# Performance work log

Measured on AMD Instinct MI355X. Metric: run time of the kernel, lower is better.

Reference implementation:

```python
import jax, jax.numpy as jnp
import numpy as np

B, T, C, H = 4, 2048, 1024, 16
D = C // H

def setup_inputs() -> dict:
    key = jax.random.key(0)
    ks = jax.random.split(key, 9)
    s = 0.02
    return {
        "x": jax.random.normal(ks[0], (B, T, C), dtype=jnp.float32),
        "Wq": jax.random.normal(ks[1], (C, C), dtype=jnp.float32) * s,
        "bq": jnp.zeros((C,), dtype=jnp.float32),
        "Wk": jax.random.normal(ks[2], (C, C), dtype=jnp.float32) * s,
        "bk": jnp.zeros((C,), dtype=jnp.float32),
        "Wv": jax.random.normal(ks[3], (C, C), dtype=jnp.float32) * s,
        "bv": jnp.zeros((C,), dtype=jnp.float32),
        "Wo": jax.random.normal(ks[4], (C, C), dtype=jnp.float32) * s,
        "bo": jnp.zeros((C,), dtype=jnp.float32),
    }

def reference(x, Wq, bq, Wk, bk, Wv, bv, Wo, bo):
    # torch nn.Linear: y = x @ W.T + b
    q = x @ Wq.T + bq  # (B,T,C)
    k = x @ Wk.T + bk
    v = x @ Wv.T + bv
    # (B,H,T,D)
    q = q.reshape(B, T, H, D).transpose(0, 2, 1, 3)
    k = k.reshape(B, T, H, D).transpose(0, 2, 1, 3)
    v = v.reshape(B, T, H, D).transpose(0, 2, 1, 3)
    scale = 1.0 / jnp.sqrt(jnp.asarray(D, dtype=q.dtype))
    att = jnp.einsum("bhqd,bhkd->bhqk", q, k) * scale  # (B,H,T,T)
    causal = jnp.tril(jnp.ones((T, T), dtype=bool))
    att = jnp.where(causal[None, None], att, jnp.asarray(-jnp.inf, dtype=att.dtype))
    att = jax.nn.softmax(att, axis=-1)
    y = jnp.einsum("bhqk,bhkd->bhqd", att, v)  # (B,H,T,D)
    y = y.transpose(0, 2, 1, 3).reshape(B, T, C)
    return y @ Wo.T + bo
```

## Files before the change

kernel.cpp:

```cpp
#include <hip/hip_runtime.h>
#include <hip/hip_bf16.h>
#include <stdint.h>

typedef unsigned short u16;
typedef __bf16 bf16x8 __attribute__((ext_vector_type(8)));
typedef float f32x4 __attribute__((ext_vector_type(4)));
typedef float f32x16 __attribute__((ext_vector_type(16)));

#define NB 4
#define NT 2048
#define NC 1024
#define NH 16
#define ND 64
#define NM 8192
#define KVB 64

__device__ __forceinline__ u16 f2bf(float f) {
  union { float f; uint32_t u; } v; v.f = f;
  return (u16)((v.u + 0x7FFFu + ((v.u >> 16) & 1u)) >> 16);
}

__device__ __forceinline__ uint32_t pk2(float a, float b) {
  union { __hip_bfloat162 h; uint32_t u; } c;
  c.h = __float22bfloat162_rn(float2{a, b});
  return c.u;
}

__device__ __forceinline__ float fexp2(float x) {
#if __has_builtin(__builtin_amdgcn_exp2f)
  return __builtin_amdgcn_exp2f(x);
#else
  return exp2f(x);
#endif
}

__device__ __forceinline__ void g2l16(const void* g, void* l) {
  __builtin_amdgcn_global_load_lds((__attribute__((address_space(1))) const void*)g,
                                   (__attribute__((address_space(3))) void*)l,
                                   16, 0, 0);
}

__global__ __launch_bounds__(256) void cvt4(const float* __restrict__ in,
                                            u16* __restrict__ out, int n4) {
  int i = blockIdx.x * 256 + threadIdx.x;
  if (i >= n4) return;
  float4 v = ((const float4*)in)[i];
  ushort4 o;
  o.x = f2bf(v.x); o.y = f2bf(v.y); o.z = f2bf(v.z); o.w = f2bf(v.w);
  ((ushort4*)out)[i] = o;
}

template <int EPI>
__global__ __launch_bounds__(512, 2) void gemmP(
    const u16* __restrict__ A,
    const u16* __restrict__ W0, const u16* __restrict__ W1, const u16* __restrict__ W2,
    const float* __restrict__ b0, const float* __restrict__ b1, const float* __restrict__ b2,
    void* o0, void* o1, void* o2, int M, int N, int K) {
  const int z = blockIdx.z;
  const u16* Bw = (z == 0) ? W0 : ((z == 1) ? W1 : W2);
  const float* bias = (z == 0) ? b0 : ((z == 1) ? b1 : b2);
  void* outp = (z == 0) ? o0 : ((z == 1) ? o1 : o2);

  __shared__ __align__(16) char SB[3 * 49152];

  const int nbn = N >> 7;
  const int lb = (blockIdx.x & 7) * (gridDim.x >> 3) + (blockIdx.x >> 3);
  const int m0 = (lb / nbn) << 8;
  const int n0 = (lb % nbn) << 7;
  const int t = threadIdx.x;
  const int wid = t >> 6, lane = t & 63;
  const int wm = wid >> 1, wn = wid & 1;
  const int lo = lane & 15, hi = lane >> 4;

  const int arow0 = t >> 3;
  const int acol = (((t & 7) ^ (arow0 & 7)) << 3);
  const u16* Asrc0 = A + (size_t)(m0 + arow0) * K + acol;
  const u16* Bsrc0 = Bw + (size_t)(n0 + arow0) * K + acol;
  const int ldsoff = t * 16;

  f32x4 acc[4][4];
#pragma unroll
  for (int f = 0; f < 4; ++f)
#pragma unroll
    for (int g = 0; g < 4; ++g) acc[f][g] = f32x4{0.f, 0.f, 0.f, 0.f};

  const int NTILES = K >> 6;

  auto STAGE = [&](int buf, int kt) {
    char* Ad = SB + buf * 49152 + ldsoff;
    char* Bd = SB + buf * 49152 + 32768 + ldsoff;
    const u16* As = Asrc0 + kt * 64;
    const u16* Bs = Bsrc0 + kt * 64;
#pragma unroll
    for (int j = 0; j < 4; ++j) g2l16(As + (size_t)(j << 6) * K, Ad + j * 8192);
#pragma unroll
    for (int j = 0; j < 2; ++j) g2l16(Bs + (size_t)(j << 6) * K, Bd + j * 8192);
  };

  STAGE(0, 0);
  STAGE(1, 1);

  int cur = 0;
  for (int kt = 0; kt < NTILES; ++kt) {
    if (kt == NTILES - 1)
      asm volatile("s_waitcnt vmcnt(0)" ::: "memory");
    else
      asm volatile("s_waitcnt vmcnt(6)" ::: "memory");
    __builtin_amdgcn_sched_barrier(0);
    __builtin_amdgcn_s_barrier();
    __builtin_amdgcn_sched_barrier(0);

    if (kt + 2 < NTILES) {
      int nb = cur + 2;
      if (nb >= 3) nb -= 3;
      STAGE(nb, kt + 2);
    }

    const char* Ab = SB + cur * 49152;
    const char* Bb = SB + cur * 49152 + 32768;
    bf16x8 af[2][4], bfr[2][4];
#pragma unroll
    for (int kh = 0; kh < 2; ++kh) {
      const int slot = ((kh << 2) | hi) ^ (lo & 7);
#pragma unroll
      for (int f = 0; f < 4; ++f)
        af[kh][f] = *(const bf16x8*)(Ab + (wm * 64 + f * 16 + lo) * 128 + slot * 16);
#pragma unroll
      for (int g = 0; g < 4; ++g)
        bfr[kh][g] = *(const bf16x8*)(Bb + (wn * 64 + g * 16 + lo) * 128 + slot * 16);
    }
    __builtin_amdgcn_s_setprio(1);
#pragma unroll
    for (int kh = 0; kh < 2; ++kh)
#pragma unroll
      for (int f = 0; f < 4; ++f)
#pragma unroll
        for (int g = 0; g < 4; ++g)
          acc[f][g] = __builtin_amdgcn_mfma_f32_16x16x32_bf16(af[kh][f], bfr[kh][g],
                                                              acc[f][g], 0, 0, 0);
    __builtin_amdgcn_s_setprio(0);
    cur = (cur + 1 == 3) ? 0 : cur + 1;
  }

  const float scl = (EPI == 0 && z == 0) ? 0.125f * 1.44269504089f : 1.0f;
#pragma unroll
  for (int f = 0; f < 4; ++f) {
#pragma unroll
    for (int g = 0; g < 4; ++g) {
#pragma unroll
      for (int r = 0; r < 4; ++r) {
        const int rg = m0 + wm * 64 + f * 16 + hi * 4 + r;
        const int cg = n0 + wn * 64 + g * 16 + lo;
        const float v = (acc[f][g][r] + bias[cg]) * scl;
        if (EPI == 0) {
          const int bb = rg >> 11, tt = rg & (NT - 1);
          const int hh = cg >> 6, dd = cg & (ND - 1);
          size_t idx;
          if (z == 2)
            idx = ((size_t)(bb * NH + hh) * ND + dd) * NT + tt;
          else
            idx = ((size_t)(bb * NH + hh) * NT + tt) * ND + dd;
          ((u16*)outp)[idx] = f2bf(v);
        } else {
          ((float*)outp)[(size_t)rg * N + cg] = v;
        }
      }
    }
  }
}

__global__ __launch_bounds__(512, 4) void flash5(const u16* __restrict__ Q,
                                                 const u16* __restrict__ Kg,
                                                 const u16* __restrict__ Vtg,
                                                 u16* __restrict__ Y) {
  __shared__ __align__(16) char LDS[65536];

  const int n = blockIdx.x;
  const int xcd = n & 7, slot = n >> 3;
  const int bh = (xcd << 3) | (slot >> 3);
  const int pt = slot & 7;
  const int qtB = 15 - pt;
  const int bb = bh >> 4, hh = bh & (NH - 1);
  const int tid = threadIdx.x;
  const int lane = tid & 63;
  const int grp = tid >> 8;
  const int ws4 = (tid >> 6) & 3;
  const int ql = lane & 31, h5 = lane >> 5;
  const int swz = (ql & 7) << 4;

  const u16* Qb = Q + (size_t)bh * NT * ND;
  const u16* Kb = Kg + (size_t)bh * NT * ND;
  const u16* Vb = Vtg + (size_t)bh * ND * NT;

  const int ntA = 2 * pt + 2;
  const int kvb1 = 15 - 2 * pt;
  const int q0wB = (qtB << 7) + (ws4 << 5);

  int q0w = grp ? q0wB : (pt << 7) + (ws4 << 5);
  int qg = q0w + ql;

  bf16x8 qf[4];
#pragma unroll
  for (int s = 0; s < 4; ++s)
    qf[s] = *(const bf16x8*)(Qb + (size_t)qg * ND + s * 16 + h5 * 8);

  f32x16 O0 = 0.f, O1 = 0.f;
  float lr = 0.f;

  const int tl = tid & 255;
  char* myL = LDS + (grp << 15);

  auto kvof = [&](int it) {
    return grp ? (kvb1 + it) : (it < ntA ? it : it - ntA);
  };

  auto STAGE = [&](int buf, int kv) {
#pragma unroll
    for (int p = 0; p < 2; ++p) {
      const int c = tl + (p << 8);
      const int row = c >> 3;
      const int so = ((c & 7) << 4) ^ ((row & 7) << 4);
      g2l16((const char*)(Kb + (size_t)((kv << 6) + row) * ND) + so,
            myL + (buf << 14) + c * 16);
      g2l16((const char*)(Vb + (size_t)row * NT + (kv << 6)) + so,
            myL + (buf << 14) + 8192 + c * 16);
    }
  };

  auto WRITEY = [&](const f32x16& A0, const f32x16& A1, float inv, int qgl) {
    u16* Yb = Y + ((size_t)bb * NT + qgl) * NC + hh * ND;
#pragma unroll
    for (int rq = 0; rq < 16; rq += 4) {
      const int dbase = 2 * rq + 4 * h5;
      uint2 w2;
      w2.x = pk2(A0[rq] * inv, A0[rq + 1] * inv);
      w2.y = pk2(A0[rq + 2] * inv, A0[rq + 3] * inv);
      *(uint2*)(Yb + dbase) = w2;
      w2.x = pk2(A1[rq] * inv, A1[rq + 1] * inv);
      w2.y = pk2(A1[rq + 2] * inv, A1[rq + 3] * inv);
      *(uint2*)(Yb + 32 + dbase) = w2;
    }
  };

  STAGE(0, kvof(0));
  __syncthreads();

  for (int it = 0; it < 17; ++it) {
    const int buf = it & 1;
    if (it < 16) STAGE(buf ^ 1, kvof(it + 1));

    if (!grp && it == ntA) {
      const float lt = lr + __shfl_xor(lr, 32, 64);
      WRITEY(O0, O1, 1.f / lt, qg);
      O0 = 0.f; O1 = 0.f; lr = 0.f;
      q0w = q0wB; qg = q0w + ql;
#pragma unroll
      for (int s = 0; s < 4; ++s)
        qf[s] = *(const bf16x8*)(Qb + (size_t)qg * ND + s * 16 + h5 * 8);
    }

    const int kv0 = kvof(it) << 6;
    const char* Kc = myL + (buf << 14);
    const char* Vc = Kc + 8192;

    f32x16 Sa0 = 0.f, Sa1 = 0.f;
    __builtin_amdgcn_s_setprio(1);
#pragma unroll
    for (int s = 0; s < 4; ++s) {
      bf16x8 kf0 = *(const bf16x8*)(Kc + ql * 128 + ((s * 32 + h5 * 16) ^ swz));
      bf16x8 kf1 = *(const bf16x8*)(Kc + (32 + ql) * 128 + ((s * 32 + h5 * 16) ^ swz));
      Sa0 = __builtin_amdgcn_mfma_f32_32x32x16_bf16(kf0, qf[s], Sa0, 0, 0, 0);
      Sa1 = __builtin_amdgcn_mfma_f32_32x32x16_bf16(kf1, qf[s], Sa1, 0, 0, 0);
    }
    __builtin_amdgcn_s_setprio(0);

    if (kv0 + 63 > q0w) {
#pragma unroll
      for (int r = 0; r < 16; ++r) {
        const int kvb = kv0 + (r & 3) + 8 * (r >> 2) + 4 * h5;
        if (kvb > qg) Sa0[r] = -3e38f;
        if (kvb + 32 > qg) Sa1[r] = -3e38f;
      }
    }

    float t0 = 0.f, t1 = 0.f, t2 = 0.f, t3 = 0.f;
#pragma unroll
    for (int r = 0; r < 16; r += 4) {
      const float a0 = fexp2(Sa0[r]),     a1 = fexp2(Sa0[r + 1]);
      const float a2 = fexp2(Sa0[r + 2]), a3 = fexp2(Sa0[r + 3]);
      const float b0 = fexp2(Sa1[r]),     b1 = fexp2(Sa1[r + 1]);
      const float b2 = fexp2(Sa1[r + 2]), b3 = fexp2(Sa1[r + 3]);
      Sa0[r] = a0; Sa0[r + 1] = a1; Sa0[r + 2] = a2; Sa0[r + 3] = a3;
      Sa1[r] = b0; Sa1[r + 1] = b1; Sa1[r + 2] = b2; Sa1[r + 3] = b3;
      t0 += a0 + b0; t1 += a1 + b1; t2 += a2 + b2; t3 += a3 + b3;
    }
    lr += (t0 + t1) + (t2 + t3);

    __builtin_amdgcn_s_setprio(1);
#pragma unroll
    for (int ks = 0; ks < 4; ++ks) {
      const int k0 = ks & 1;
      const f32x16& Sk = (ks < 2) ? Sa0 : Sa1;
      const uint32_t a0 = pk2(Sk[8 * k0],     Sk[8 * k0 + 1]);
      const uint32_t a1 = pk2(Sk[8 * k0 + 2], Sk[8 * k0 + 3]);
      const uint32_t b0 = pk2(Sk[8 * k0 + 4], Sk[8 * k0 + 5]);
      const uint32_t b1 = pk2(Sk[8 * k0 + 6], Sk[8 * k0 + 7]);
      const uint32_t c0 = h5 ? b0 : a0, c1 = h5 ? b1 : a1;
      const uint32_t d0 = h5 ? a0 : b0, d1 = h5 ? a1 : b1;
      const uint32_t x0 = __shfl_xor(d0, 32, 64);
      const uint32_t x1 = __shfl_xor(d1, 32, 64);
      union { uint32_t u[4]; bf16x8 v; } pf;
      pf.u[0] = h5 ? x0 : c0;
      pf.u[1] = h5 ? x1 : c1;
      pf.u[2] = h5 ? c0 : x0;
      pf.u[3] = h5 ? c1 : x1;
      bf16x8 vf0 = *(const bf16x8*)(Vc + ql * 128 + ((ks * 32 + h5 * 16) ^ swz));
      bf16x8 vf1 = *(const bf16x8*)(Vc + (32 + ql) * 128 + ((ks * 32 + h5 * 16) ^ swz));
      O0 = __builtin_amdgcn_mfma_f32_32x32x16_bf16(vf0, pf.v, O0, 0, 0, 0);
      O1 = __builtin_amdgcn_mfma_f32_32x32x16_bf16(vf1, pf.v, O1, 0, 0, 0);
    }
    __builtin_amdgcn_s_setprio(0);

    __syncthreads();
  }

  const int cslot = (ws4 << 6) + lane;
  char* cb = LDS + cslot * 136;
  if (!grp) {
#pragma unroll
    for (int j = 0; j < 8; ++j) {
      *(float2*)(cb + j * 8)      = float2{O0[2 * j], O0[2 * j + 1]};
      *(float2*)(cb + 64 + j * 8) = float2{O1[2 * j], O1[2 * j + 1]};
    }
    *(float*)(cb + 128) = lr;
  }
  __syncthreads();
  if (grp) {
#pragma unroll
    for (int j = 0; j < 8; ++j) {
      const float2 u = *(const float2*)(cb + j * 8);
      const float2 v = *(const float2*)(cb + 64 + j * 8);
      O0[2 * j] += u.x; O0[2 * j + 1] += u.y;
      O1[2 * j] += v.x; O1[2 * j + 1] += v.y;
    }
    lr += *(const float*)(cb + 128);
    const float lt = lr + __shfl_xor(lr, 32, 64);
    WRITEY(O0, O1, 1.f / lt, qg);
  }
}

extern "C" void kernel_launch(void* const* d_in, const int* in_sizes, int n_in,
                              void* d_out, int out_size, void* d_ws, size_t ws_size,
                              hipStream_t stream) {
  const float* x  = (const float*)d_in[0];
  const float* Wq = (const float*)d_in[1];
  const float* bq = (const float*)d_in[2];
  const float* Wk = (const float*)d_in[3];
  const float* bk = (const float*)d_in[4];
  const float* Wv = (const float*)d_in[5];
  const float* bv = (const float*)d_in[6];
  const float* Wo = (const float*)d_in[7];
  const float* bo = (const float*)d_in[8];

  const size_t SZ_X = (size_t)NM * NC * 2;
  const size_t SZ_W = (size_t)NC * NC * 2;
  char* ws = (char*)d_ws;
  u16* xb  = (u16*)ws;
  u16* wqb = (u16*)(ws + SZ_X);
  u16* wkb = (u16*)(ws + SZ_X + 1 * SZ_W);
  u16* wvb = (u16*)(ws + SZ_X + 2 * SZ_W);
  u16* wob = (u16*)(ws + SZ_X + 3 * SZ_W);
  u16* vb  = (u16*)(ws + SZ_X + 4 * SZ_W);
  u16* yb  = (u16*)(ws + 2 * SZ_X + 4 * SZ_W);
  u16* qb = (u16*)d_out;
  u16* kb = (u16*)((char*)d_out + SZ_X);

  if (ws_size < 3 * SZ_X + 4 * SZ_W) return;

  cvt4<<<dim3(NM * NC / 4 / 256), 256, 0, stream>>>(x, xb, NM * NC / 4);
  cvt4<<<dim3(NC * NC / 4 / 256), 256, 0, stream>>>(Wq, wqb, NC * NC / 4);
  cvt4<<<dim3(NC * NC / 4 / 256), 256, 0, stream>>>(Wk, wkb, NC * NC / 4);
  cvt4<<<dim3(NC * NC / 4 / 256), 256, 0, stream>>>(Wv, wvb, NC * NC / 4);
  cvt4<<<dim3(NC * NC / 4 / 256), 256, 0, stream>>>(Wo, wob, NC * NC / 4);

  gemmP<0><<<dim3(256, 1, 3), 512, 0, stream>>>(
      xb, wqb, wkb, wvb, bq, bk, bv, qb, kb, vb, NM, NC, NC);

  flash5<<<dim3(512), 512, 0, stream>>>(qb, kb, vb, yb);

  gemmP<1><<<dim3(256, 1, 1), 512, 0, stream>>>(
      yb, wob, wob, wob, bo, bo, bo, d_out, d_out, d_out, NM, NC, NC);
}
```

Baseline: 165.5 us.

## Interleave async LDS prefetch with two k-half MFMA phases and flatten QKV grid

The GEMM main loop is split into two k-half phases separated by an extra barrier. Each phase issues half of the next-next tile's global-to-LDS loads right after its own LDS fragment reads, so global traffic is spread across the MFMA work instead of issued in one burst. The QKV projection grid is also flattened from a 3D launch into a 1D grid of 768 blocks, with the weight matrix (z) folded into the XCD-swizzled tile index so all three projections share A-tile locality. K and N become compile-time constants. The extra barrier per tile adds synchronization cost.

Result: slower. 171.1 us (+3.4%).

```diff
diff --git a/kernel.cpp b/kernel.cpp
--- a/kernel.cpp
+++ b/kernel.cpp
@@ -51,22 +51,24 @@
 }
 
 template <int EPI>
-__global__ __launch_bounds__(512, 2) void gemmP(
+__global__ __launch_bounds__(512, 2) void gemmF(
     const u16* __restrict__ A,
     const u16* __restrict__ W0, const u16* __restrict__ W1, const u16* __restrict__ W2,
     const float* __restrict__ b0, const float* __restrict__ b1, const float* __restrict__ b2,
-    void* o0, void* o1, void* o2, int M, int N, int K) {
-  const int z = blockIdx.z;
+    void* o0, void* o1, void* o2) {
+  constexpr int K = NC;
+  __shared__ __align__(16) char SB[3 * 49152];
+
+  const int ntn = gridDim.x >> 5;
+  const int lb = (blockIdx.x & 7) * (gridDim.x >> 3) + (blockIdx.x >> 3);
+  const int m0 = (lb / ntn) << 8;
+  const int nt = lb % ntn;
+  const int z = nt >> 3;
+  const int n0 = (nt & 7) << 7;
   const u16* Bw = (z == 0) ? W0 : ((z == 1) ? W1 : W2);
   const float* bias = (z == 0) ? b0 : ((z == 1) ? b1 : b2);
   void* outp = (z == 0) ? o0 : ((z == 1) ? o1 : o2);
 
-  __shared__ __align__(16) char SB[3 * 49152];
-
-  const int nbn = N >> 7;
-  const int lb = (blockIdx.x & 7) * (gridDim.x >> 3) + (blockIdx.x >> 3);
-  const int m0 = (lb / nbn) << 8;
-  const int n0 = (lb % nbn) << 7;
   const int t = threadIdx.x;
   const int wid = t >> 6, lane = t & 63;
   const int wm = wid >> 1, wn = wid & 1;
@@ -86,7 +88,7 @@
 
   const int NTILES = K >> 6;
 
-  auto STAGE = [&](int buf, int kt) {
+  auto STAGE_FULL = [&](int buf, int kt) {
     char* Ad = SB + buf * 49152 + ldsoff;
     char* Bd = SB + buf * 49152 + 32768 + ldsoff;
     const u16* As = Asrc0 + kt * 64;
@@ -97,8 +99,8 @@
     for (int j = 0; j < 2; ++j) g2l16(Bs + (size_t)(j << 6) * K, Bd + j * 8192);
   };
 
-  STAGE(0, 0);
-  STAGE(1, 1);
+  STAGE_FULL(0, 0);
+  STAGE_FULL(1, 1);
 
   int cur = 0;
   for (int kt = 0; kt < NTILES; ++kt) {
@@ -107,38 +109,69 @@
     else
       asm volatile("s_waitcnt vmcnt(6)" ::: "memory");
     __builtin_amdgcn_sched_barrier(0);
-    __builtin_amdgcn_s_barrier();
+    asm volatile("s_barrier" ::: "memory");
     __builtin_amdgcn_sched_barrier(0);
-
-    if (kt + 2 < NTILES) {
-      int nb = cur + 2;
-      if (nb >= 3) nb -= 3;
-      STAGE(nb, kt + 2);
-    }
 
     const char* Ab = SB + cur * 49152;
     const char* Bb = SB + cur * 49152 + 32768;
-    bf16x8 af[2][4], bfr[2][4];
-#pragma unroll
-    for (int kh = 0; kh < 2; ++kh) {
-      const int slot = ((kh << 2) | hi) ^ (lo & 7);
+    int nb = cur + 2;
+    if (nb >= 3) nb -= 3;
+    char* Ad = SB + nb * 49152 + ldsoff;
+    char* Bd = SB + nb * 49152 + 32768 + ldsoff;
+    const u16* As = Asrc0 + (kt + 2) * 64;
+    const u16* Bs = Bsrc0 + (kt + 2) * 64;
+    const bool st = (kt + 2 < NTILES);
+
+    {
+      const int ksl = 0;
+      const int slot = ((ksl << 2) | hi) ^ (lo & 7);
+      bf16x8 af[4], bfr[4];
 #pragma unroll
       for (int f = 0; f < 4; ++f)
-        af[kh][f] = *(const bf16x8*)(Ab + (wm * 64 + f * 16 + lo) * 128 + slot * 16);
+        af[f] = *(const bf16x8*)(Ab + (wm * 64 + f * 16 + lo) * 128 + slot * 16);
 #pragma unroll
       for (int g = 0; g < 4; ++g)
-        bfr[kh][g] = *(const bf16x8*)(Bb + (wn * 64 + g * 16 + lo) * 128 + slot * 16);
-    }
-    __builtin_amdgcn_s_setprio(1);
-#pragma unroll
-    for (int kh = 0; kh < 2; ++kh)
+        bfr[g] = *(const bf16x8*)(Bb + (wn * 64 + g * 16 + lo) * 128 + slot * 16);
+      if (st) {
+        g2l16(As + (size_t)(0 << 6) * K, Ad + 0 * 8192);
+        g2l16(As + (size_t)(1 << 6) * K, Ad + 1 * 8192);
+        g2l16(Bs + (size_t)(0 << 6) * K, Bd + 0 * 8192);
+      }
+      __builtin_amdgcn_s_setprio(1);
 #pragma unroll
       for (int f = 0; f < 4; ++f)
 #pragma unroll
         for (int g = 0; g < 4; ++g)
-          acc[f][g] = __builtin_amdgcn_mfma_f32_16x16x32_bf16(af[kh][f], bfr[kh][g],
+          acc[f][g] = __builtin_amdgcn_mfma_f32_16x16x32_bf16(af[f], bfr[g],
                                                               acc[f][g], 0, 0, 0);
-    __builtin_amdgcn_s_setprio(0);
+      __builtin_amdgcn_s_setprio(0);
+    }
+    asm volatile("s_barrier" ::: "memory");
+
+    {
+      const int ksl = 1;
+      const int slot = ((ksl << 2) | hi) ^ (lo & 7);
+      bf16x8 af[4], bfr[4];
+#pragma unroll
+      for (int f = 0; f < 4; ++f)
+        af[f] = *(const bf16x8*)(Ab + (wm * 64 + f * 16 + lo) * 128 + slot * 16);
+#pragma unroll
+      for (int g = 0; g < 4; ++g)
+        bfr[g] = *(const bf16x8*)(Bb + (wn * 64 + g * 16 + lo) * 128 + slot * 16);
+      if (st) {
+        g2l16(As + (size_t)(2 << 6) * K, Ad + 2 * 8192);
+        g2l16(As + (size_t)(3 << 6) * K, Ad + 3 * 8192);
+        g2l16(Bs + (size_t)(1 << 6) * K, Bd + 1 * 8192);
+      }
+      __builtin_amdgcn_s_setprio(1);
+#pragma unroll
+      for (int f = 0; f < 4; ++f)
+#pragma unroll
+        for (int g = 0; g < 4; ++g)
+          acc[f][g] = __builtin_amdgcn_mfma_f32_16x16x32_bf16(af[f], bfr[g],
+                                                              acc[f][g], 0, 0, 0);
+      __builtin_amdgcn_s_setprio(0);
+    }
     cur = (cur + 1 == 3) ? 0 : cur + 1;
   }
 
@@ -162,7 +195,7 @@
             idx = ((size_t)(bb * NH + hh) * NT + tt) * ND + dd;
           ((u16*)outp)[idx] = f2bf(v);
         } else {
-          ((float*)outp)[(size_t)rg * N + cg] = v;
+          ((float*)outp)[(size_t)rg * NC + cg] = v;
         }
       }
     }
@@ -383,11 +416,11 @@
   cvt4<<<dim3(NC * NC / 4 / 256), 256, 0, stream>>>(Wv, wvb, NC * NC / 4);
   cvt4<<<dim3(NC * NC / 4 / 256), 256, 0, stream>>>(Wo, wob, NC * NC / 4);
 
-  gemmP<0><<<dim3(256, 1, 3), 512, 0, stream>>>(
-      xb, wqb, wkb, wvb, bq, bk, bv, qb, kb, vb, NM, NC, NC);
+  gemmF<0><<<dim3(768), 512, 0, stream>>>(
+      xb, wqb, wkb, wvb, bq, bk, bv, qb, kb, vb);
 
   flash5<<<dim3(512), 512, 0, stream>>>(qb, kb, vb, yb);
 
-  gemmP<1><<<dim3(256, 1, 1), 512, 0, stream>>>(
-      yb, wob, wob, wob, bo, bo, bo, d_out, d_out, d_out, NM, NC, NC);
-}
+  gemmF<1><<<dim3(256), 512, 0, stream>>>(
+      yb, wob, wob, wob, bo, bo, bo, d_out, d_out, d_out);
+}
```

## Shrink GEMM tiles to 128x128x32 for higher occupancy and merge weight conversions

Applied to the files above, without the earlier changes.

The projection GEMMs move from 256x128 tiles with K-step 64 (144KB LDS, 2 blocks/CU) to 128x128 tiles with K-step 32 (48KB LDS), using a 2x4 wave layout, a new XOR swizzle, and twice as many blocks. The goal is more resident blocks per CU and better load balance across the grid, so that latency is hidden through occupancy. The cost is less data reuse per tile and more barriers per unit of work. Separately, the four weight-conversion launches become one kernel with a 2D grid, which removes launch overhead.

Result: slower. 171.3 us (+3.5%).

```diff
diff --git a/kernel.cpp b/kernel.cpp
--- a/kernel.cpp
+++ b/kernel.cpp
@@ -50,8 +50,23 @@
   ((ushort4*)out)[i] = o;
 }
 
+__global__ __launch_bounds__(256) void cvtW(const float* __restrict__ w0,
+                                            const float* __restrict__ w1,
+                                            const float* __restrict__ w2,
+                                            const float* __restrict__ w3,
+                                            u16* o0, u16* o1, u16* o2, u16* o3) {
+  const int y = blockIdx.y;
+  const float* in = (y == 0) ? w0 : (y == 1) ? w1 : (y == 2) ? w2 : w3;
+  u16* out = (y == 0) ? o0 : (y == 1) ? o1 : (y == 2) ? o2 : o3;
+  int i = blockIdx.x * 256 + threadIdx.x;
+  float4 v = ((const float4*)in)[i];
+  ushort4 o;
+  o.x = f2bf(v.x); o.y = f2bf(v.y); o.z = f2bf(v.z); o.w = f2bf(v.w);
+  ((ushort4*)out)[i] = o;
+}
+
 template <int EPI>
-__global__ __launch_bounds__(512, 2) void gemmP(
+__global__ __launch_bounds__(512, 6) void gemmQ(
     const u16* __restrict__ A,
     const u16* __restrict__ W0, const u16* __restrict__ W1, const u16* __restrict__ W2,
     const float* __restrict__ b0, const float* __restrict__ b1, const float* __restrict__ b2,
@@ -61,40 +76,34 @@
   const float* bias = (z == 0) ? b0 : ((z == 1) ? b1 : b2);
   void* outp = (z == 0) ? o0 : ((z == 1) ? o1 : o2);
 
-  __shared__ __align__(16) char SB[3 * 49152];
+  __shared__ __align__(16) char SB[3 * 16384];
 
   const int nbn = N >> 7;
   const int lb = (blockIdx.x & 7) * (gridDim.x >> 3) + (blockIdx.x >> 3);
-  const int m0 = (lb / nbn) << 8;
+  const int m0 = (lb / nbn) << 7;
   const int n0 = (lb % nbn) << 7;
   const int t = threadIdx.x;
   const int wid = t >> 6, lane = t & 63;
-  const int wm = wid >> 1, wn = wid & 1;
+  const int wm = wid >> 2, wn = wid & 3;
   const int lo = lane & 15, hi = lane >> 4;
 
-  const int arow0 = t >> 3;
-  const int acol = (((t & 7) ^ (arow0 & 7)) << 3);
-  const u16* Asrc0 = A + (size_t)(m0 + arow0) * K + acol;
-  const u16* Bsrc0 = Bw + (size_t)(n0 + arow0) * K + acol;
+  const int rw = t >> 2;
+  const int chs = (((t & 3) ^ (rw & 3) ^ ((rw >> 2) & 3)) << 3);
+  const u16* Asrc0 = A + (size_t)(m0 + rw) * K + chs;
+  const u16* Bsrc0 = Bw + (size_t)(n0 + rw) * K + chs;
   const int ldsoff = t * 16;
 
-  f32x4 acc[4][4];
+  f32x4 acc[4][2];
 #pragma unroll
   for (int f = 0; f < 4; ++f)
 #pragma unroll
-    for (int g = 0; g < 4; ++g) acc[f][g] = f32x4{0.f, 0.f, 0.f, 0.f};
-
-  const int NTILES = K >> 6;
+    for (int g = 0; g < 2; ++g) acc[f][g] = f32x4{0.f, 0.f, 0.f, 0.f};
+
+  const int NTILES = K >> 5;
 
   auto STAGE = [&](int buf, int kt) {
-    char* Ad = SB + buf * 49152 + ldsoff;
-    char* Bd = SB + buf * 49152 + 32768 + ldsoff;
-    const u16* As = Asrc0 + kt * 64;
-    const u16* Bs = Bsrc0 + kt * 64;
-#pragma unroll
-    for (int j = 0; j < 4; ++j) g2l16(As + (size_t)(j << 6) * K, Ad + j * 8192);
-#pragma unroll
-    for (int j = 0; j < 2; ++j) g2l16(Bs + (size_t)(j << 6) * K, Bd + j * 8192);
+    g2l16(Asrc0 + kt * 32, SB + buf * 16384 + ldsoff);
+    g2l16(Bsrc0 + kt * 32, SB + buf * 16384 + 8192 + ldsoff);
   };
 
   STAGE(0, 0);
@@ -105,9 +114,9 @@
     if (kt == NTILES - 1)
       asm volatile("s_waitcnt vmcnt(0)" ::: "memory");
     else
-      asm volatile("s_waitcnt vmcnt(6)" ::: "memory");
+      asm volatile("s_waitcnt vmcnt(2)" ::: "memory");
     __builtin_amdgcn_sched_barrier(0);
-    __builtin_amdgcn_s_barrier();
+    asm volatile("s_barrier" ::: "memory");
     __builtin_amdgcn_sched_barrier(0);
 
     if (kt + 2 < NTILES) {
@@ -116,28 +125,26 @@
       STAGE(nb, kt + 2);
     }
 
-    const char* Ab = SB + cur * 49152;
-    const char* Bb = SB + cur * 49152 + 32768;
-    bf16x8 af[2][4], bfr[2][4];
-#pragma unroll
-    for (int kh = 0; kh < 2; ++kh) {
-      const int slot = ((kh << 2) | hi) ^ (lo & 7);
-#pragma unroll
-      for (int f = 0; f < 4; ++f)
-        af[kh][f] = *(const bf16x8*)(Ab + (wm * 64 + f * 16 + lo) * 128 + slot * 16);
-#pragma unroll
-      for (int g = 0; g < 4; ++g)
-        bfr[kh][g] = *(const bf16x8*)(Bb + (wn * 64 + g * 16 + lo) * 128 + slot * 16);
+    const char* Ab = SB + cur * 16384;
+    const char* Bb = SB + cur * 16384 + 8192;
+    bf16x8 af[4], bfr[2];
+#pragma unroll
+    for (int f = 0; f < 4; ++f) {
+      const int row = wm * 64 + f * 16 + lo;
+      af[f] = *(const bf16x8*)(Ab + row * 64 + ((hi ^ (row & 3) ^ ((row >> 2) & 3)) << 4));
+    }
+#pragma unroll
+    for (int g = 0; g < 2; ++g) {
+      const int row = wn * 32 + g * 16 + lo;
+      bfr[g] = *(const bf16x8*)(Bb + row * 64 + ((hi ^ (row & 3) ^ ((row >> 2) & 3)) << 4));
     }
     __builtin_amdgcn_s_setprio(1);
 #pragma unroll
-    for (int kh = 0; kh < 2; ++kh)
-#pragma unroll
-      for (int f = 0; f < 4; ++f)
-#pragma unroll
-        for (int g = 0; g < 4; ++g)
-          acc[f][g] = __builtin_amdgcn_mfma_f32_16x16x32_bf16(af[kh][f], bfr[kh][g],
-                                                              acc[f][g], 0, 0, 0);
+    for (int f = 0; f < 4; ++f)
+#pragma unroll
+      for (int g = 0; g < 2; ++g)
+        acc[f][g] = __builtin_amdgcn_mfma_f32_16x16x32_bf16(af[f], bfr[g],
+                                                            acc[f][g], 0, 0, 0);
     __builtin_amdgcn_s_setprio(0);
     cur = (cur + 1 == 3) ? 0 : cur + 1;
   }
@@ -146,11 +153,11 @@
 #pragma unroll
   for (int f = 0; f < 4; ++f) {
 #pragma unroll
-    for (int g = 0; g < 4; ++g) {
+    for (int g = 0; g < 2; ++g) {
 #pragma unroll
       for (int r = 0; r < 4; ++r) {
         const int rg = m0 + wm * 64 + f * 16 + hi * 4 + r;
-        const int cg = n0 + wn * 64 + g * 16 + lo;
+        const int cg = n0 + wn * 32 + g * 16 + lo;
         const float v = (acc[f][g][r] + bias[cg]) * scl;
         if (EPI == 0) {
           const int bb = rg >> 11, tt = rg & (NT - 1);
@@ -378,16 +385,14 @@
   if (ws_size < 3 * SZ_X + 4 * SZ_W) return;
 
   cvt4<<<dim3(NM * NC / 4 / 256), 256, 0, stream>>>(x, xb, NM * NC / 4);
-  cvt4<<<dim3(NC * NC / 4 / 256), 256, 0, stream>>>(Wq, wqb, NC * NC / 4);
-  cvt4<<<dim3(NC * NC / 4 / 256), 256, 0, stream>>>(Wk, wkb, NC * NC / 4);
-  cvt4<<<dim3(NC * NC / 4 / 256), 256, 0, stream>>>(Wv, wvb, NC * NC / 4);
-  cvt4<<<dim3(NC * NC / 4 / 256), 256, 0, stream>>>(Wo, wob, NC * NC / 4);
-
-  gemmP<0><<<dim3(256, 1, 3), 512, 0, stream>>>(
+  cvtW<<<dim3(NC * NC / 4 / 256, 4), 256, 0, stream>>>(Wq, Wk, Wv, Wo,
+                                                       wqb, wkb, wvb, wob);
+
+  gemmQ<0><<<dim3(512, 1, 3), 512, 0, stream>>>(
       xb, wqb, wkb, wvb, bq, bk, bv, qb, kb, vb, NM, NC, NC);
 
   flash5<<<dim3(512), 512, 0, stream>>>(qb, kb, vb, yb);
 
-  gemmP<1><<<dim3(256, 1, 1), 512, 0, stream>>>(
+  gemmQ<1><<<dim3(512, 1, 1), 512, 0, stream>>>(
       yb, wob, wob, wob, bo, bo, bo, d_out, d_out, d_out, NM, NC, NC);
 }
```
